# Performance work log

Measured on AMD Instinct MI355X. Metric: run time of the kernel, lower is better.

## Reference

```python
import jax, jax.numpy as jnp
import numpy as np

H = 14
N = H * H
DIM = 768
INT = 5
LAM = 3.5


def fft_conv_grouped(x, w):
    # x: (B, g*in_c, N) real; w: (g, int_c, in_c, H, H//2+1) complex
    g, int_c, in_c = w.shape[:3]
    B = x.shape[0]
    xf = jnp.fft.rfftn(x.reshape(B, g, in_c, H, H), axes=(-2, -1), norm='ortho')
    yf = jnp.einsum('bgchf,gichf->bgihf', xf, w)
    y = jnp.fft.irfftn(yf, s=(H, H), axes=(-2, -1), norm='ortho')
    return y.reshape(B, g * int_c, N)


def soft(x, t):
    # sign(x) * relu(|x| - t)
    return jnp.sign(x) * jnp.maximum(jnp.abs(x) - t, 0.0)


def batch_norm(x, gamma, beta, eps=1e-5):
    # training-mode BatchNorm1d applied per channel over (B, N); x: (B, N, C)
    m = x.mean(axis=(0, 1))
    v = x.var(axis=(0, 1))
    return (x - m) * jax.lax.rsqrt(v + eps) * gamma + beta


def setup_inputs() -> dict:
    key = jax.random.key(0)
    ks = jax.random.split(key, 8)
    B = 32
    Hf = H // 2 + 1
    # kernel: init randn*0.06, then normalize_parameters()
    kr = jax.random.normal(ks[0], (DIM, INT, 1, H, Hf, 2), dtype=jnp.float32) * 0.06
    kc = kr[..., 0] + 1j * kr[..., 1]
    nrm = jnp.sqrt((jnp.abs(kc) ** 2).sum(axis=(2, 3, 4), keepdims=True) * 2.0 / H ** 2)
    kc = kc / nrm
    kernel = jnp.stack([jnp.real(kc), jnp.imag(kc)], axis=-1)
    # L buffer: update_L(lam=1) -> per-group max singular value of Gram kk
    kk = jnp.einsum('gichf,gjchf->gijhf', kc, jnp.conj(kc))
    sv = np.linalg.svd(np.asarray(jnp.transpose(kk, (0, 3, 4, 1, 2))), compute_uv=False)
    L = jnp.asarray(sv.reshape(DIM, -1).max(axis=-1), dtype=jnp.float32)
    hid = 4 * DIM
    return {
        'x': jax.random.normal(ks[1], (B, N, DIM), dtype=jnp.float32),
        'v_w': jax.random.normal(ks[2], (DIM, DIM), dtype=jnp.float32) * 0.02,
        'proj_w': jax.random.normal(ks[3], (DIM, DIM), dtype=jnp.float32) * 0.02,
        'proj_b': jnp.zeros((DIM,), dtype=jnp.float32),
        'kernel': kernel,
        'kernel2': jax.random.normal(ks[4], (DIM, 1, 1, H, Hf, 2), dtype=jnp.float32) * 0.02,
        'n1_g': jnp.ones((DIM,), dtype=jnp.float32),
        'n1_b': jnp.zeros((DIM,), dtype=jnp.float32),
        'n2_g': jnp.ones((DIM,), dtype=jnp.float32),
        'n2_b': jnp.zeros((DIM,), dtype=jnp.float32),
        'fc1_w': jax.random.normal(ks[5], (hid, DIM), dtype=jnp.float32) * 0.02,
        'fc1_b': jnp.zeros((hid,), dtype=jnp.float32),
        'fc2_w': jax.random.normal(ks[6], (DIM, hid), dtype=jnp.float32) * 0.02,
        'fc2_b': jnp.zeros((DIM,), dtype=jnp.float32),
        'L': L,
    }


def reference(x, v_w, proj_w, proj_b, kernel, kernel2, n1_g, n1_b, n2_g, n2_b, fc1_w, fc1_b, fc2_w, fc2_b, L):
    k = kernel[..., 0] + 1j * kernel[..., 1]                 # (g, int, 1, H, Hf)
    kk = jnp.einsum('gichf,gjchf->gijhf', k, jnp.conj(k))     # (g, int, int, H, Hf)
    vx = x @ v_w.T                                            # v Linear, no bias
    xc = jnp.swapaxes(vx, -2, -1)                             # (B, C, N)
    u = fft_conv_grouped(xc, k)                               # (B, g*int, N)
    Lv = jnp.repeat(L, INT)[None, :, None]                    # (1, g*int, 1)
    # ISTA: init soft-threshold then 3 gradient + shrink steps
    s = soft(u, LAM)
    for _ in range(3):
        s = s - (fft_conv_grouped(s, kk) - u) / Lv
        s = soft(s, LAM / Lv)
    # reconstruct with conjugate-transposed kernel, then mix with kernel2
    new = fft_conv_grouped(s, jnp.swapaxes(jnp.conj(k), 1, 2))  # (B, g, N)
    k2 = kernel2[..., 0] + 1j * kernel2[..., 1]
    new = fft_conv_grouped(new, k2)
    new = jnp.swapaxes(new, -2, -1)                           # (B, N, C)
    new = x + (batch_norm(new, n1_g, n1_b) @ proj_w.T + proj_b)
    h = jax.nn.gelu(batch_norm(new, n2_g, n2_b) @ fc1_w.T + fc1_b, approximate=False)
    return new + (h @ fc2_w.T + fc2_b)
```

## Files before the change

### kernel.cpp

```cpp
#include <hip/hip_runtime.h>
#include <cmath>

typedef unsigned short u16;
typedef __bf16 bf16x8 __attribute__((ext_vector_type(8)));
typedef float f32x4 __attribute__((ext_vector_type(4)));
typedef float float4v __attribute__((ext_vector_type(4)));
typedef u16 ushort4v __attribute__((ext_vector_type(4)));
typedef u16 ushort8v __attribute__((ext_vector_type(8)));

#define DIMC 768
#define NP 196
#define MTOT 6272
#define HIDC 3072
#define LAMC 3.5f

__device__ const float C14d[14] = {
  1.0f, 0.9009688679024191f, 0.6234898018587336f, 0.22252093395631445f,
  -0.22252093395631445f, -0.6234898018587336f, -0.9009688679024191f, -1.0f,
  -0.9009688679024191f, -0.6234898018587336f, -0.22252093395631445f,
  0.22252093395631445f, 0.6234898018587336f, 0.9009688679024191f
};
__device__ const float S14d[14] = {
  0.0f, 0.43388373911755823f, 0.7818314824680298f, 0.9749279121818236f,
  0.9749279121818236f, 0.7818314824680298f, 0.43388373911755823f, 0.0f,
  -0.43388373911755823f, -0.7818314824680298f, -0.9749279121818236f,
  -0.9749279121818236f, -0.7818314824680298f, -0.43388373911755823f
};

__device__ __forceinline__ u16 f2bf(float f) {
  unsigned u = __builtin_bit_cast(unsigned, f);
  unsigned r = u + 0x7FFFu + ((u >> 16) & 1u);
  return (u16)(r >> 16);
}

typedef const __attribute__((address_space(1))) u16* gas_p;
typedef __attribute__((address_space(3))) u16* las_p;
__device__ __forceinline__ void gl16(const u16* g, u16* l) {
  __builtin_amdgcn_global_load_lds((gas_p)g, (las_p)l, 16, 0, 0);
}

__global__ __launch_bounds__(256) void initfg_k(u16* __restrict__ Ff, u16* __restrict__ Gf) {
  int idx = blockIdx.x * 256 + threadIdx.x;
  if (idx < 50176) {
    int j = idx & 7, lane = (idx >> 3) & 63;
    int mk = idx >> 9, k0 = mk % 7, m0 = mk / 7;
    int s = m0 * 16 + (lane & 15);
    int q = k0 * 32 + (lane >> 4) * 8 + j;
    float v = 0.f;
    if (q < 196) {
      int kr = s >> 4, f = (s >> 1) & 7, r = q / 14, c = q % 14;
      int th = (kr * r + f * c) % 14;
      v = (s & 1) ? -S14d[th] : C14d[th];
    }
    Ff[idx] = f2bf(v);
  } else if (idx < 50176 + 46592) {
    int t = idx - 50176;
    int j = t & 7, lane = (t >> 3) & 63;
    int pk = t >> 9, k0 = pk % 7, p0 = pk / 7;
    int p = p0 * 16 + (lane & 15);
    int s = k0 * 32 + (lane >> 4) * 8 + j;
    float v = 0.f;
    if (p < 196) {
      int kr = s >> 4, f = (s >> 1) & 7, r = p / 14, c = p % 14;
      int th = (kr * r + f * c) % 14;
      float w = (f == 0 || f == 7) ? 1.f : 2.f;
      v = (w * (1.f / 196.f)) * ((s & 1) ? -S14d[th] : C14d[th]);
    }
    Gf[t] = f2bf(v);
  }
}

__global__ __launch_bounds__(256) void cvtw_k(
    const float* __restrict__ w0, const float* __restrict__ w1,
    const float* __restrict__ w2, const float* __restrict__ w3,
    u16* __restrict__ o0, u16* __restrict__ o1,
    u16* __restrict__ o2, u16* __restrict__ o3) {
  int idx = blockIdx.x * 256 + threadIdx.x;
  const float* s; u16* d; int base;
  if (idx < 147456)      { s = w0; d = o0; base = 0; }
  else if (idx < 294912) { s = w1; d = o1; base = 147456; }
  else if (idx < 884736) { s = w2; d = o2; base = 294912; }
  else                   { s = w3; d = o3; base = 884736; }
  int i4 = (idx - base) * 4;
  float4v v = *(const float4v*)(s + i4);
  ushort4v o;
#pragma unroll
  for (int j = 0; j < 4; ++j) o[j] = f2bf(v[j]);
  *(ushort4v*)(d + i4) = o;
}

__global__ __launch_bounds__(256) void cvt4_k(const float* __restrict__ s,
                                              u16* __restrict__ d, int n4) {
  int idx = blockIdx.x * 256 + threadIdx.x;
  if (idx >= n4) return;
  int i4 = idx * 4;
  float4v v = *(const float4v*)(s + i4);
  ushort4v o;
#pragma unroll
  for (int j = 0; j < 4; ++j) o[j] = f2bf(v[j]);
  *(ushort4v*)(d + i4) = o;
}

__global__ __launch_bounds__(256) void bncvt_k(const float* __restrict__ s,
    const float* __restrict__ sc, const float* __restrict__ sh,
    u16* __restrict__ d, int n4) {
  int idx = blockIdx.x * 256 + threadIdx.x;
  if (idx >= n4) return;
  int i4 = idx * 4;
  int c = i4 % DIMC;
  float4v v = *(const float4v*)(s + i4);
  float4v a = *(const float4v*)(sc + c);
  float4v b = *(const float4v*)(sh + c);
  v = v * a + b;
  ushort4v o;
#pragma unroll
  for (int j = 0; j < 4; ++j) o[j] = f2bf(v[j]);
  *(ushort4v*)(d + i4) = o;
}

template<int EPI>
__global__ __launch_bounds__(256) void gemm_k(
    const u16* __restrict__ A, const u16* __restrict__ Bw,
    const float* __restrict__ bias, const float* __restrict__ res,
    void* __restrict__ Cp, int Nr, int Kr) {
  __shared__ __attribute__((aligned(16))) u16 As[128 * 32];
  __shared__ __attribute__((aligned(16))) u16 Bs[128 * 32];
  const int t = threadIdx.x;
  const int wid = t >> 6, lane = t & 63;
  const int bn = blockIdx.x * 128, bm = blockIdx.y * 128;
  const int wm = (wid >> 1) * 64, wn = (wid & 1) * 64;
  const int l15 = lane & 15, l4 = lane >> 4;
  const int srow = lane >> 2, scol = (lane & 3) * 8;

  f32x4 acc[4][4];
#pragma unroll
  for (int a = 0; a < 4; ++a)
#pragma unroll
    for (int b2 = 0; b2 < 4; ++b2) acc[a][b2] = (f32x4){0.f, 0.f, 0.f, 0.f};

  const u16* gA0 = A + (size_t)(bm + wid * 16 + srow) * Kr + scol;
  const u16* gB0 = Bw + (size_t)(bn + wid * 16 + srow) * Kr + scol;
  u16* lA = As + wid * 512;
  u16* lB = Bs + wid * 512;

  for (int k0 = 0; k0 < Kr; k0 += 32) {
    gl16(gA0 + k0, lA);
    gl16(gA0 + (size_t)64 * Kr + k0, lA + 2048);
    gl16(gB0 + k0, lB);
    gl16(gB0 + (size_t)64 * Kr + k0, lB + 2048);
    __syncthreads();

    bf16x8 af[4], bfv[4];
#pragma unroll
    for (int mb = 0; mb < 4; ++mb)
      af[mb] = *(const bf16x8*)&As[(wm + mb * 16 + l15) * 32 + l4 * 8];
#pragma unroll
    for (int nb = 0; nb < 4; ++nb)
      bfv[nb] = *(const bf16x8*)&Bs[(wn + nb * 16 + l15) * 32 + l4 * 8];
#pragma unroll
    for (int mb = 0; mb < 4; ++mb)
#pragma unroll
      for (int nb = 0; nb < 4; ++nb)
        acc[mb][nb] = __builtin_amdgcn_mfma_f32_16x16x32_bf16(af[mb], bfv[nb], acc[mb][nb], 0, 0, 0);
    __syncthreads();
  }

#pragma unroll
  for (int mb = 0; mb < 4; ++mb) {
#pragma unroll
    for (int nb = 0; nb < 4; ++nb) {
      int n = bn + wn + nb * 16 + l15;
#pragma unroll
      for (int r = 0; r < 4; ++r) {
        int m = bm + wm + mb * 16 + l4 * 4 + r;
        float v = acc[mb][nb][r];
        if (EPI == 0) {
          int bb = m / 196, np = m - bb * 196;
          ((float*)Cp)[((size_t)bb * DIMC + n) * 196 + np] = v;
        } else if (EPI == 1) {
          ((float*)Cp)[(size_t)m * Nr + n] = v + bias[n] + res[(size_t)m * Nr + n];
        } else {
          float vb = v + bias[n];
          float ge = 0.5f * vb * (1.f + erff(vb * 0.70710678118654752f));
          ((u16*)Cp)[(size_t)m * Nr + n] = f2bf(ge);
        }
      }
    }
  }
}

__global__ __launch_bounds__(256) void stats_part_k(const float* __restrict__ A,
                                                    float* __restrict__ part) {
  int blk = blockIdx.x, t = threadIdx.x;
  float s0a = 0, s0b = 0, s0c = 0, s1a = 0, s1b = 0, s1c = 0;
  const float* base = A + (size_t)blk * 64 * DIMC;
  for (int r = 0; r < 64; ++r) {
    const float* row = base + (size_t)r * DIMC;
    float v0 = row[t], v1 = row[t + 256], v2 = row[t + 512];
    s0a += v0; s1a += v0 * v0;
    s0b += v1; s1b += v1 * v1;
    s0c += v2; s1c += v2 * v2;
  }
  part[(size_t)blk * DIMC + t] = s0a;
  part[(size_t)blk * DIMC + t + 256] = s0b;
  part[(size_t)blk * DIMC + t + 512] = s0c;
  float* p2 = part + 98 * DIMC;
  p2[(size_t)blk * DIMC + t] = s1a;
  p2[(size_t)blk * DIMC + t + 256] = s1b;
  p2[(size_t)blk * DIMC + t + 512] = s1c;
}

__global__ __launch_bounds__(256) void stats_fin_k(const float* __restrict__ part,
    const float* __restrict__ gam, const float* __restrict__ bet,
    float* __restrict__ scale, float* __restrict__ shift) {
  int c = blockIdx.x * 256 + threadIdx.x;
  if (c >= DIMC) return;
  float S = 0.f, Q = 0.f;
  for (int b = 0; b < 98; ++b) {
    S += part[(size_t)b * DIMC + c];
    Q += part[(size_t)(98 + b) * DIMC + c];
  }
  float m = S * (1.0f / 6272.0f);
  float v = Q * (1.0f / 6272.0f) - m * m;
  v = fmaxf(v, 0.f);
  float rs = rsqrtf(v + 1e-5f);
  float sc = gam[c] * rs;
  scale[c] = sc;
  shift[c] = bet[c] - m * sc;
}

__global__ __launch_bounds__(64) void checkmfma_k(
    const float* __restrict__ vxt, const float* __restrict__ kern,
    const u16* __restrict__ Ff, const u16* __restrict__ Gf,
    int* __restrict__ cnt, int* __restrict__ wl) {
  __shared__ float xf[16 * 228];
  const int lane = threadIdx.x;
  const int wgb = blockIdx.x;
  const int g = wgb >> 1, bhalf = wgb & 1;
  const int tl = lane & 15, h = lane >> 4;
  const float* xbase = vxt + ((size_t)(bhalf * 16 + tl) * DIMC + g) * 196;

  bf16x8 Bx[7];
#pragma unroll
  for (int k0 = 0; k0 < 7; ++k0) {
    int q0 = k0 * 32 + h * 8;
    ushort8v tv;
    if (k0 < 6) {
      float4v f0 = *(const float4v*)(xbase + q0);
      float4v f1 = *(const float4v*)(xbase + q0 + 4);
#pragma unroll
      for (int j = 0; j < 4; ++j) { tv[j] = f2bf(f0[j]); tv[j + 4] = f2bf(f1[j]); }
    } else {
#pragma unroll
      for (int j = 0; j < 8; ++j) {
        int q = q0 + j;
        tv[j] = (q < 196) ? f2bf(xbase[q]) : (u16)0;
      }
    }
    Bx[k0] = __builtin_bit_cast(bf16x8, tv);
  }

  for (int m0 = 0; m0 < 14; ++m0) {
    f32x4 acc = (f32x4){0.f, 0.f, 0.f, 0.f};
#pragma unroll
    for (int k0 = 0; k0 < 7; ++k0) {
      bf16x8 Af = __builtin_bit_cast(bf16x8,
          *(const ushort8v*)(Ff + ((size_t)(m0 * 7 + k0) * 64 + lane) * 8));
      acc = __builtin_amdgcn_mfma_f32_16x16x32_bf16(Af, Bx[k0], acc, 0, 0, 0);
    }
    *(f32x4*)&xf[tl * 228 + m0 * 16 + h * 4] = acc;
  }

  bf16x8 By[5][7];
#pragma unroll
  for (int i = 0; i < 5; ++i) {
    const float* kb = kern + ((size_t)g * 5 + i) * 224;
#pragma unroll
    for (int k0 = 0; k0 < 7; ++k0) {
      f32x4 x0 = *(const f32x4*)&xf[tl * 228 + k0 * 32 + h * 8];
      f32x4 x1 = *(const f32x4*)&xf[tl * 228 + k0 * 32 + h * 8 + 4];
      int mb = k0 * 16 + h * 4;
      float2 ka = *(const float2*)(kb + (mb + 0) * 2);
      float2 kc = *(const float2*)(kb + (mb + 1) * 2);
      float2 ke = *(const float2*)(kb + (mb + 2) * 2);
      float2 kg = *(const float2*)(kb + (mb + 3) * 2);
      ushort8v tv;
      tv[0] = f2bf(ka.x * x0[0] - ka.y * x0[1]);
      tv[1] = f2bf(ka.x * x0[1] + ka.y * x0[0]);
      tv[2] = f2bf(kc.x * x0[2] - kc.y * x0[3]);
      tv[3] = f2bf(kc.x * x0[3] + kc.y * x0[2]);
      tv[4] = f2bf(ke.x * x1[0] - ke.y * x1[1]);
      tv[5] = f2bf(ke.x * x1[1] + ke.y * x1[0]);
      tv[6] = f2bf(kg.x * x1[0 + 2] - kg.y * x1[3]);
      tv[7] = f2bf(kg.x * x1[3] + kg.y * x1[2]);
      By[i][k0] = __builtin_bit_cast(bf16x8, tv);
    }
  }

  float vmax = 0.f;
  for (int p0 = 0; p0 < 13; ++p0) {
    f32x4 a0 = (f32x4){0.f, 0.f, 0.f, 0.f};
    f32x4 a1 = a0, a2 = a0, a3 = a0, a4 = a0;
#pragma unroll
    for (int k0 = 0; k0 < 7; ++k0) {
      bf16x8 Ag = __builtin_bit_cast(bf16x8,
          *(const ushort8v*)(Gf + ((size_t)(p0 * 7 + k0) * 64 + lane) * 8));
      a0 = __builtin_amdgcn_mfma_f32_16x16x32_bf16(Ag, By[0][k0], a0, 0, 0, 0);
      a1 = __builtin_amdgcn_mfma_f32_16x16x32_bf16(Ag, By[1][k0], a1, 0, 0, 0);
      a2 = __builtin_amdgcn_mfma_f32_16x16x32_bf16(Ag, By[2][k0], a2, 0, 0, 0);
      a3 = __builtin_amdgcn_mfma_f32_16x16x32_bf16(Ag, By[3][k0], a3, 0, 0, 0);
      a4 = __builtin_amdgcn_mfma_f32_16x16x32_bf16(Ag, By[4][k0], a4, 0, 0, 0);
    }
#pragma unroll
    for (int r = 0; r < 4; ++r) {
      vmax = fmaxf(vmax, fabsf(a0[r]));
      vmax = fmaxf(vmax, fabsf(a1[r]));
      vmax = fmaxf(vmax, fabsf(a2[r]));
      vmax = fmaxf(vmax, fabsf(a3[r]));
      vmax = fmaxf(vmax, fabsf(a4[r]));
    }
  }
  vmax = fmaxf(vmax, __shfl_xor(vmax, 16));
  vmax = fmaxf(vmax, __shfl_xor(vmax, 32));
  if (lane < 16 && vmax > (LAMC - 0.1f)) {
    int idx = atomicAdd(cnt, 1);
    wl[idx] = g * 32 + bhalf * 16 + lane;
  }
}

__global__ __launch_bounds__(64) void slow_k(
    const float* __restrict__ vxt, const float* __restrict__ kern,
    const float* __restrict__ kern2, const float* __restrict__ Lbuf,
    const int* __restrict__ cnt, const int* __restrict__ wl,
    float* __restrict__ outp) {
  const int t = threadIdx.x;
  __shared__ float TC[196], TSn[196];
  __shared__ float xs[196];
  __shared__ float t1R[112], t1I[112];
  __shared__ float t2R[112], t2I[112];
  __shared__ float zr[112], zi[112];
  __shared__ float kR[5][112], kI[5][112];
  __shared__ float uu[5][196];
  __shared__ float ss[5][196];
  __shared__ float k2R[112], k2I[112];

  for (int i = t; i < 196; i += 64) {
    int a = i / 14, c = i - (i / 14) * 14;
    int m = (a * c) % 14;
    TC[i] = C14d[m]; TSn[i] = S14d[m];
  }
  const int ntile = *cnt;

  auto rowsFwd = [&](const float* xsrc) {
    for (int i = t; i < 112; i += 64) {
      int r = i >> 3, f = i & 7;
      const float* xp = xsrc + r * 14;
      const float* tc = &TC[f * 14]; const float* tsn = &TSn[f * 14];
      float ar = 0.f, ai = 0.f;
#pragma unroll
      for (int c = 0; c < 14; ++c) { float xv = xp[c]; ar += xv * tc[c]; ai -= xv * tsn[c]; }
      t1R[i] = ar; t1I[i] = ai;
    }
    __syncthreads();
  };
  auto colsFwd = [&](float* oR, float* oI) {
    for (int i = t; i < 112; i += 64) {
      int kr = i >> 3, f = i & 7;
      const float* tc = &TC[kr * 14]; const float* tsn = &TSn[kr * 14];
      float br = 0.f, bi = 0.f;
#pragma unroll
      for (int r = 0; r < 14; ++r) {
        float xr = t1R[r * 8 + f], xi = t1I[r * 8 + f];
        br += tc[r] * xr + tsn[r] * xi;
        bi += tc[r] * xi - tsn[r] * xr;
      }
      oR[i] = br; oI[i] = bi;
    }
    __syncthreads();
  };
  auto colsInv = [&]() {
    for (int i = t; i < 112; i += 64) {
      int r = i >> 3, f = i & 7;
      const float* tc = &TC[r * 14]; const float* tsn = &TSn[r * 14];
      float br = 0.f, bi = 0.f;
#pragma unroll
      for (int kr = 0; kr < 14; ++kr) {
        float xr = t1R[kr * 8 + f], xi = t1I[kr * 8 + f];
        br += tc[kr] * xr - tsn[kr] * xi;
        bi += tc[kr] * xi + tsn[kr] * xr;
      }
      t2R[i] = br; t2I[i] = bi;
    }
    __syncthreads();
  };
  auto rowVal = [&](int r, int c) -> float {
    const float* pR = &t2R[r * 8]; const float* pI = &t2I[r * 8];
    float v = pR[0] + ((c & 1) ? -pR[7] : pR[7]);
    float s2 = 0.f;
#pragma unroll
    for (int f = 1; f < 7; ++f) s2 += pR[f] * TC[f * 14 + c] - pI[f] * TSn[f * 14 + c];
    return (v + 2.f * s2) * (1.0f / 196.0f);
  };

  for (int widx = blockIdx.x; widx < ntile; widx += gridDim.x) {
    const int tile = wl[widx];
    const int g = tile >> 5, b = tile & 31;
    __syncthreads();
    for (int i = t; i < 560; i += 64) {
      int ii = i / 112, p = i - ii * 112;
      const float* kp = kern + ((size_t)g * 5 + ii) * 224 + p * 2;
      kR[ii][p] = kp[0]; kI[ii][p] = kp[1];
    }
    for (int i = t; i < 196; i += 64) xs[i] = vxt[((size_t)b * DIMC + g) * 196 + i];
    for (int i = t; i < 112; i += 64) {
      k2R[i] = kern2[(size_t)g * 224 + i * 2];
      k2I[i] = kern2[(size_t)g * 224 + i * 2 + 1];
    }
    __syncthreads();

    rowsFwd(xs);
    colsFwd(zr, zi);
    for (int ii = 0; ii < 5; ++ii) {
      for (int i = t; i < 112; i += 64) {
        float a = kR[ii][i], b2 = kI[ii][i];
        t1R[i] = a * zr[i] - b2 * zi[i];
        t1I[i] = a * zi[i] + b2 * zr[i];
      }
      __syncthreads();
      colsInv();
      for (int i = t; i < 196; i += 64) uu[ii][i] = rowVal(i / 14, i - (i / 14) * 14);
      __syncthreads();
    }

    const float invL = 1.0f / Lbuf[g];
    const float thr = LAMC * invL;
    {
      float* up = &uu[0][0];
      float* sp = &ss[0][0];
      for (int i = t; i < 980; i += 64) {
        float v = up[i];
        float a = fabsf(v) - LAMC;
        sp[i] = a > 0.f ? copysignf(a, v) : 0.f;
      }
    }
    __syncthreads();

    for (int iter = 0; iter < 4; ++iter) {
      for (int i = t; i < 112; i += 64) { zr[i] = 0.f; zi[i] = 0.f; }
      __syncthreads();
      for (int ii = 0; ii < 5; ++ii) {
        rowsFwd(&ss[ii][0]);
        colsFwd(t2R, t2I);
        for (int i = t; i < 112; i += 64) {
          float a = kR[ii][i], b2 = kI[ii][i];
          zr[i] += a * t2R[i] + b2 * t2I[i];
          zi[i] += a * t2I[i] - b2 * t2R[i];
        }
        __syncthreads();
      }
      if (iter == 3) break;
      for (int ii = 0; ii < 5; ++ii) {
        for (int i = t; i < 112; i += 64) {
          float a = kR[ii][i], b2 = kI[ii][i];
          t1R[i] = a * zr[i] - b2 * zi[i];
          t1I[i] = a * zi[i] + b2 * zr[i];
        }
        __syncthreads();
        colsInv();
        for (int i = t; i < 196; i += 64) {
          float v = rowVal(i / 14, i - (i / 14) * 14);
          float sv = ss[ii][i] - (v - uu[ii][i]) * invL;
          float aa = fabsf(sv) - thr;
          ss[ii][i] = aa > 0.f ? copysignf(aa, sv) : 0.f;
        }
        __syncthreads();
      }
    }

    if (t < 28) {
      int kr = t >> 1, f = (t & 1) * 7;
      int d = kr * 8 + f;
      int srci = ((14 - kr) % 14) * 8 + f;
      float pr = 0.5f * (zr[d] + zr[srci]);
      float pi = 0.5f * (zi[d] - zi[srci]);
      zr[d] = pr; zi[d] = pi;
    }
    __syncthreads();
    for (int i = t; i < 112; i += 64) {
      float a = k2R[i], b2 = k2I[i];
      t1R[i] = a * zr[i] - b2 * zi[i];
      t1I[i] = a * zi[i] + b2 * zr[i];
    }
    __syncthreads();
    colsInv();
    for (int i = t; i < 196; i += 64)
      outp[((size_t)(b * 196 + i)) * DIMC + g] = rowVal(i / 14, i - (i / 14) * 14);
  }
}

extern "C" void kernel_launch(void* const* d_in, const int* in_sizes, int n_in,
                              void* d_out, int out_size, void* d_ws, size_t ws_size,
                              hipStream_t stream) {
  (void)in_sizes; (void)n_in; (void)out_size;
  const float* x      = (const float*)d_in[0];
  const float* v_w    = (const float*)d_in[1];
  const float* proj_w = (const float*)d_in[2];
  const float* proj_b = (const float*)d_in[3];
  const float* kern   = (const float*)d_in[4];
  const float* kern2  = (const float*)d_in[5];
  const float* n1g    = (const float*)d_in[6];
  const float* n1b    = (const float*)d_in[7];
  const float* n2g    = (const float*)d_in[8];
  const float* n2b    = (const float*)d_in[9];
  const float* fc1w   = (const float*)d_in[10];
  const float* fc1b   = (const float*)d_in[11];
  const float* fc2w   = (const float*)d_in[12];
  const float* fc2b   = (const float*)d_in[13];
  const float* Lb     = (const float*)d_in[14];
  float* out = (float*)d_out;

  char* ws = (char*)d_ws;
  size_t o = 0;
  auto alloc = [&](size_t bytes) { size_t r = o; o += (bytes + 255) & ~(size_t)255; return r; };
  u16*   vwbf   = (u16*)(ws + alloc(589824 * 2));
  u16*   projbf = (u16*)(ws + alloc(589824 * 2));
  u16*   fc1bf  = (u16*)(ws + alloc(2359296 * 2));
  u16*   fc2bf  = (u16*)(ws + alloc(2359296 * 2));
  u16*   Ffb    = (u16*)(ws + alloc(50176 * 2));
  u16*   Gfb    = (u16*)(ws + alloc(46592 * 2));
  float* sc1    = (float*)(ws + alloc(768 * 4));
  float* sh1    = (float*)(ws + alloc(768 * 4));
  float* sc2    = (float*)(ws + alloc(768 * 4));
  float* sh2    = (float*)(ws + alloc(768 * 4));
  float* part   = (float*)(ws + alloc(98 * 768 * 2 * 4));
  int*   cnt    = (int*)(ws + alloc(4));
  int*   wl     = (int*)(ws + alloc(24576 * 4));
  u16*   abf    = (u16*)(ws + alloc((size_t)MTOT * DIMC * 2));
  float* vxt    = (float*)(ws + alloc((size_t)MTOT * DIMC * 4));
  float* newm   = (float*)(ws + alloc((size_t)MTOT * DIMC * 4));
  float* new2   = (float*)(ws + alloc((size_t)MTOT * DIMC * 4));
  u16*   hbf    = (u16*)vxt;
  if (ws_size < o) return;

  hipMemsetAsync(newm, 0, (size_t)MTOT * DIMC * 4, stream);
  hipMemsetAsync(cnt, 0, 4, stream);

  initfg_k<<<378, 256, 0, stream>>>(Ffb, Gfb);
  cvtw_k<<<5760, 256, 0, stream>>>(v_w, proj_w, fc1w, fc2w, vwbf, projbf, fc1bf, fc2bf);
  cvt4_k<<<4704, 256, 0, stream>>>(x, abf, 1204224);

  gemm_k<0><<<dim3(6, 49), 256, 0, stream>>>(abf, vwbf, nullptr, nullptr, vxt, DIMC, DIMC);
  checkmfma_k<<<1536, 64, 0, stream>>>(vxt, kern, Ffb, Gfb, cnt, wl);
  slow_k<<<1024, 64, 0, stream>>>(vxt, kern, kern2, Lb, cnt, wl, newm);
  stats_part_k<<<98, 256, 0, stream>>>(newm, part);
  stats_fin_k<<<3, 256, 0, stream>>>(part, n1g, n1b, sc1, sh1);
  bncvt_k<<<4704, 256, 0, stream>>>(newm, sc1, sh1, abf, 1204224);
  gemm_k<1><<<dim3(6, 49), 256, 0, stream>>>(abf, projbf, proj_b, x, new2, DIMC, DIMC);
  stats_part_k<<<98, 256, 0, stream>>>(new2, part);
  stats_fin_k<<<3, 256, 0, stream>>>(part, n2g, n2b, sc2, sh2);
  bncvt_k<<<4704, 256, 0, stream>>>(new2, sc2, sh2, abf, 1204224);
  gemm_k<2><<<dim3(24, 49), 256, 0, stream>>>(abf, fc1bf, fc1b, nullptr, hbf, HIDC, DIMC);
  gemm_k<1><<<dim3(6, 49), 256, 0, stream>>>(hbf, fc2bf, fc2b, new2, out, DIMC, HIDC);
}
```

Measured before the change: 333.8 us.

## Split-K the fc2 GEMM with bf16 partials and store LDS tiles in fragment order

```diff
diff --git a/kernel.cpp b/kernel.cpp
--- a/kernel.cpp
+++ b/kernel.cpp
@@ -31,6 +31,9 @@
   unsigned u = __builtin_bit_cast(unsigned, f);
   unsigned r = u + 0x7FFFu + ((u >> 16) & 1u);
   return (u16)(r >> 16);
+}
+__device__ __forceinline__ float bf2f(u16 u) {
+  return __builtin_bit_cast(float, (unsigned)u << 16);
 }
 
 typedef const __attribute__((address_space(1))) u16* gas_p;
@@ -118,19 +121,19 @@
   *(ushort4v*)(d + i4) = o;
 }
 
-template<int EPI>
+template<int EPI, int SPLIT = 0>
 __global__ __launch_bounds__(256) void gemm_k(
     const u16* __restrict__ A, const u16* __restrict__ Bw,
     const float* __restrict__ bias, const float* __restrict__ res,
-    void* __restrict__ Cp, int Nr, int Kr) {
+    void* __restrict__ Cp, int Nr, int Kr, int ld) {
   __shared__ __attribute__((aligned(16))) u16 As[128 * 32];
   __shared__ __attribute__((aligned(16))) u16 Bs[128 * 32];
   const int t = threadIdx.x;
   const int wid = t >> 6, lane = t & 63;
   const int bn = blockIdx.x * 128, bm = blockIdx.y * 128;
+  const int kz = SPLIT ? blockIdx.z : 0;
   const int wm = (wid >> 1) * 64, wn = (wid & 1) * 64;
   const int l15 = lane & 15, l4 = lane >> 4;
-  const int srow = lane >> 2, scol = (lane & 3) * 8;
 
   f32x4 acc[4][4];
 #pragma unroll
@@ -138,25 +141,25 @@
 #pragma unroll
     for (int b2 = 0; b2 < 4; ++b2) acc[a][b2] = (f32x4){0.f, 0.f, 0.f, 0.f};
 
-  const u16* gA0 = A + (size_t)(bm + wid * 16 + srow) * Kr + scol;
-  const u16* gB0 = Bw + (size_t)(bn + wid * 16 + srow) * Kr + scol;
+  const u16* gA0 = A + (size_t)(bm + wid * 16 + l15) * ld + (size_t)kz * Kr + l4 * 8;
+  const u16* gB0 = Bw + (size_t)(bn + wid * 16 + l15) * ld + (size_t)kz * Kr + l4 * 8;
   u16* lA = As + wid * 512;
   u16* lB = Bs + wid * 512;
 
   for (int k0 = 0; k0 < Kr; k0 += 32) {
     gl16(gA0 + k0, lA);
-    gl16(gA0 + (size_t)64 * Kr + k0, lA + 2048);
+    gl16(gA0 + (size_t)64 * ld + k0, lA + 2048);
     gl16(gB0 + k0, lB);
-    gl16(gB0 + (size_t)64 * Kr + k0, lB + 2048);
+    gl16(gB0 + (size_t)64 * ld + k0, lB + 2048);
     __syncthreads();
 
     bf16x8 af[4], bfv[4];
 #pragma unroll
     for (int mb = 0; mb < 4; ++mb)
-      af[mb] = *(const bf16x8*)&As[(wm + mb * 16 + l15) * 32 + l4 * 8];
+      af[mb] = *(const bf16x8*)&As[((wid >> 1) * 4 + mb) * 512 + lane * 8];
 #pragma unroll
     for (int nb = 0; nb < 4; ++nb)
-      bfv[nb] = *(const bf16x8*)&Bs[(wn + nb * 16 + l15) * 32 + l4 * 8];
+      bfv[nb] = *(const bf16x8*)&Bs[((wid & 1) * 4 + nb) * 512 + lane * 8];
 #pragma unroll
     for (int mb = 0; mb < 4; ++mb)
 #pragma unroll
@@ -179,14 +182,36 @@
           ((float*)Cp)[((size_t)bb * DIMC + n) * 196 + np] = v;
         } else if (EPI == 1) {
           ((float*)Cp)[(size_t)m * Nr + n] = v + bias[n] + res[(size_t)m * Nr + n];
-        } else {
+        } else if (EPI == 2) {
           float vb = v + bias[n];
           float ge = 0.5f * vb * (1.f + erff(vb * 0.70710678118654752f));
           ((u16*)Cp)[(size_t)m * Nr + n] = f2bf(ge);
+        } else {
+          ((u16*)Cp)[(size_t)kz * MTOT * DIMC + (size_t)m * Nr + n] = f2bf(v);
         }
       }
     }
   }
+}
+
+__global__ __launch_bounds__(256) void redc_k(const u16* __restrict__ p,
+    const float* __restrict__ bias, const float* __restrict__ res,
+    float* __restrict__ out) {
+  int idx = blockIdx.x * 256 + threadIdx.x;
+  size_t i4 = (size_t)idx * 4;
+  const size_t S = (size_t)MTOT * DIMC;
+  ushort4v p0 = *(const ushort4v*)(p + i4);
+  ushort4v p1 = *(const ushort4v*)(p + S + i4);
+  ushort4v p2 = *(const ushort4v*)(p + 2 * S + i4);
+  ushort4v p3 = *(const ushort4v*)(p + 3 * S + i4);
+  float4v r = *(const float4v*)(res + i4);
+  int c = (int)(i4 % DIMC);
+  float4v bs = *(const float4v*)(bias + c);
+  float4v o;
+#pragma unroll
+  for (int j = 0; j < 4; ++j)
+    o[j] = bf2f(p0[j]) + bf2f(p1[j]) + bf2f(p2[j]) + bf2f(p3[j]) + bs[j] + r[j];
+  *(float4v*)(out + i4) = o;
 }
 
 __global__ __launch_bounds__(256) void stats_part_k(const float* __restrict__ A,
@@ -291,7 +316,7 @@
       tv[3] = f2bf(kc.x * x0[3] + kc.y * x0[2]);
       tv[4] = f2bf(ke.x * x1[0] - ke.y * x1[1]);
       tv[5] = f2bf(ke.x * x1[1] + ke.y * x1[0]);
-      tv[6] = f2bf(kg.x * x1[0 + 2] - kg.y * x1[3]);
+      tv[6] = f2bf(kg.x * x1[2] - kg.y * x1[3]);
       tv[7] = f2bf(kg.x * x1[3] + kg.y * x1[2]);
       By[i][k0] = __builtin_bit_cast(bf16x8, tv);
     }
@@ -539,6 +564,7 @@
   float* vxt    = (float*)(ws + alloc((size_t)MTOT * DIMC * 4));
   float* newm   = (float*)(ws + alloc((size_t)MTOT * DIMC * 4));
   float* new2   = (float*)(ws + alloc((size_t)MTOT * DIMC * 4));
+  u16*   pbf    = (u16*)(ws + alloc((size_t)4 * MTOT * DIMC * 2));
   u16*   hbf    = (u16*)vxt;
   if (ws_size < o) return;
 
@@ -549,16 +575,17 @@
   cvtw_k<<<5760, 256, 0, stream>>>(v_w, proj_w, fc1w, fc2w, vwbf, projbf, fc1bf, fc2bf);
   cvt4_k<<<4704, 256, 0, stream>>>(x, abf, 1204224);
 
-  gemm_k<0><<<dim3(6, 49), 256, 0, stream>>>(abf, vwbf, nullptr, nullptr, vxt, DIMC, DIMC);
+  gemm_k<0><<<dim3(6, 49), 256, 0, stream>>>(abf, vwbf, nullptr, nullptr, vxt, DIMC, DIMC, DIMC);
   checkmfma_k<<<1536, 64, 0, stream>>>(vxt, kern, Ffb, Gfb, cnt, wl);
   slow_k<<<1024, 64, 0, stream>>>(vxt, kern, kern2, Lb, cnt, wl, newm);
   stats_part_k<<<98, 256, 0, stream>>>(newm, part);
   stats_fin_k<<<3, 256, 0, stream>>>(part, n1g, n1b, sc1, sh1);
   bncvt_k<<<4704, 256, 0, stream>>>(newm, sc1, sh1, abf, 1204224);
-  gemm_k<1><<<dim3(6, 49), 256, 0, stream>>>(abf, projbf, proj_b, x, new2, DIMC, DIMC);
+  gemm_k<1><<<dim3(6, 49), 256, 0, stream>>>(abf, projbf, proj_b, x, new2, DIMC, DIMC, DIMC);
   stats_part_k<<<98, 256, 0, stream>>>(new2, part);
   stats_fin_k<<<3, 256, 0, stream>>>(part, n2g, n2b, sc2, sh2);
   bncvt_k<<<4704, 256, 0, stream>>>(new2, sc2, sh2, abf, 1204224);
-  gemm_k<2><<<dim3(24, 49), 256, 0, stream>>>(abf, fc1bf, fc1b, nullptr, hbf, HIDC, DIMC);
-  gemm_k<1><<<dim3(6, 49), 256, 0, stream>>>(hbf, fc2bf, fc2b, new2, out, DIMC, HIDC);
-}
+  gemm_k<2><<<dim3(24, 49), 256, 0, stream>>>(abf, fc1bf, fc1b, nullptr, hbf, HIDC, DIMC, DIMC);
+  gemm_k<3, 1><<<dim3(6, 49, 4), 256, 0, stream>>>(hbf, fc2bf, nullptr, nullptr, pbf, DIMC, 768, HIDC);
+  redc_k<<<4704, 256, 0, stream>>>(pbf, fc2b, new2, out);
+}
```

Result: slower. 365.3 us (+9.4%).

## Double-buffer GEMM LDS tiles, store fragments in MFMA order, vectorize transposed epilogue

Applied to the files above, without the earlier changes.

```diff
diff --git a/kernel.cpp b/kernel.cpp
--- a/kernel.cpp
+++ b/kernel.cpp
@@ -31,6 +31,9 @@
   unsigned u = __builtin_bit_cast(unsigned, f);
   unsigned r = u + 0x7FFFu + ((u >> 16) & 1u);
   return (u16)(r >> 16);
+}
+__device__ __forceinline__ float bf2f(u16 u) {
+  return __builtin_bit_cast(float, (unsigned)u << 16);
 }
 
 typedef const __attribute__((address_space(1))) u16* gas_p;
@@ -122,15 +125,14 @@
 __global__ __launch_bounds__(256) void gemm_k(
     const u16* __restrict__ A, const u16* __restrict__ Bw,
     const float* __restrict__ bias, const float* __restrict__ res,
-    void* __restrict__ Cp, int Nr, int Kr) {
-  __shared__ __attribute__((aligned(16))) u16 As[128 * 32];
-  __shared__ __attribute__((aligned(16))) u16 Bs[128 * 32];
+    void* __restrict__ Cp, int Nr, int Kr, int ld) {
+  __shared__ __attribute__((aligned(16))) u16 As[2][128 * 32];
+  __shared__ __attribute__((aligned(16))) u16 Bs[2][128 * 32];
   const int t = threadIdx.x;
   const int wid = t >> 6, lane = t & 63;
   const int bn = blockIdx.x * 128, bm = blockIdx.y * 128;
   const int wm = (wid >> 1) * 64, wn = (wid & 1) * 64;
   const int l15 = lane & 15, l4 = lane >> 4;
-  const int srow = lane >> 2, scol = (lane & 3) * 8;
 
   f32x4 acc[4][4];
 #pragma unroll
@@ -138,31 +140,40 @@
 #pragma unroll
     for (int b2 = 0; b2 < 4; ++b2) acc[a][b2] = (f32x4){0.f, 0.f, 0.f, 0.f};
 
-  const u16* gA0 = A + (size_t)(bm + wid * 16 + srow) * Kr + scol;
-  const u16* gB0 = Bw + (size_t)(bn + wid * 16 + srow) * Kr + scol;
-  u16* lA = As + wid * 512;
-  u16* lB = Bs + wid * 512;
+  const u16* gA0 = A + (size_t)(bm + wid * 16 + l15) * ld + l4 * 8;
+  const u16* gB0 = Bw + (size_t)(bn + wid * 16 + l15) * ld + l4 * 8;
+
+  auto STAGE = [&](int buf, int k0) {
+    u16* lA = &As[buf][wid * 512];
+    u16* lB = &Bs[buf][wid * 512];
+    gl16(gA0 + k0, lA);
+    gl16(gA0 + (size_t)64 * ld + k0, lA + 2048);
+    gl16(gB0 + k0, lB);
+    gl16(gB0 + (size_t)64 * ld + k0, lB + 2048);
+  };
+
+  STAGE(0, 0);
+  __syncthreads();
+  int cur = 0;
 
   for (int k0 = 0; k0 < Kr; k0 += 32) {
-    gl16(gA0 + k0, lA);
-    gl16(gA0 + (size_t)64 * Kr + k0, lA + 2048);
-    gl16(gB0 + k0, lB);
-    gl16(gB0 + (size_t)64 * Kr + k0, lB + 2048);
-    __syncthreads();
+    if (k0 + 32 < Kr) STAGE(cur ^ 1, k0 + 32);
 
     bf16x8 af[4], bfv[4];
 #pragma unroll
     for (int mb = 0; mb < 4; ++mb)
-      af[mb] = *(const bf16x8*)&As[(wm + mb * 16 + l15) * 32 + l4 * 8];
+      af[mb] = *(const bf16x8*)&As[cur][((wid >> 1) * 4 + mb) * 512 + lane * 8];
 #pragma unroll
     for (int nb = 0; nb < 4; ++nb)
-      bfv[nb] = *(const bf16x8*)&Bs[(wn + nb * 16 + l15) * 32 + l4 * 8];
+      bfv[nb] = *(const bf16x8*)&Bs[cur][((wid & 1) * 4 + nb) * 512 + lane * 8];
 #pragma unroll
     for (int mb = 0; mb < 4; ++mb)
 #pragma unroll
       for (int nb = 0; nb < 4; ++nb)
         acc[mb][nb] = __builtin_amdgcn_mfma_f32_16x16x32_bf16(af[mb], bfv[nb], acc[mb][nb], 0, 0, 0);
-    __syncthreads();
+
+    __syncthreads();
+    cur ^= 1;
   }
 
 #pragma unroll
@@ -170,19 +181,23 @@
 #pragma unroll
     for (int nb = 0; nb < 4; ++nb) {
       int n = bn + wn + nb * 16 + l15;
-#pragma unroll
-      for (int r = 0; r < 4; ++r) {
-        int m = bm + wm + mb * 16 + l4 * 4 + r;
-        float v = acc[mb][nb][r];
-        if (EPI == 0) {
-          int bb = m / 196, np = m - bb * 196;
-          ((float*)Cp)[((size_t)bb * DIMC + n) * 196 + np] = v;
-        } else if (EPI == 1) {
-          ((float*)Cp)[(size_t)m * Nr + n] = v + bias[n] + res[(size_t)m * Nr + n];
-        } else {
-          float vb = v + bias[n];
-          float ge = 0.5f * vb * (1.f + erff(vb * 0.70710678118654752f));
-          ((u16*)Cp)[(size_t)m * Nr + n] = f2bf(ge);
+      if (EPI == 0) {
+        int m0 = bm + wm + mb * 16 + l4 * 4;
+        int bb = m0 / 196, np0 = m0 - bb * 196;
+        *(float4v*)&((float*)Cp)[((size_t)bb * DIMC + n) * 196 + np0] =
+            (float4v){acc[mb][nb][0], acc[mb][nb][1], acc[mb][nb][2], acc[mb][nb][3]};
+      } else {
+#pragma unroll
+        for (int r = 0; r < 4; ++r) {
+          int m = bm + wm + mb * 16 + l4 * 4 + r;
+          float v = acc[mb][nb][r];
+          if (EPI == 1) {
+            ((float*)Cp)[(size_t)m * Nr + n] = v + bias[n] + res[(size_t)m * Nr + n];
+          } else {
+            float vb = v + bias[n];
+            float ge = 0.5f * vb * (1.f + erff(vb * 0.70710678118654752f));
+            ((u16*)Cp)[(size_t)m * Nr + n] = f2bf(ge);
+          }
         }
       }
     }
@@ -291,7 +306,7 @@
       tv[3] = f2bf(kc.x * x0[3] + kc.y * x0[2]);
       tv[4] = f2bf(ke.x * x1[0] - ke.y * x1[1]);
       tv[5] = f2bf(ke.x * x1[1] + ke.y * x1[0]);
-      tv[6] = f2bf(kg.x * x1[0 + 2] - kg.y * x1[3]);
+      tv[6] = f2bf(kg.x * x1[2] - kg.y * x1[3]);
       tv[7] = f2bf(kg.x * x1[3] + kg.y * x1[2]);
       By[i][k0] = __builtin_bit_cast(bf16x8, tv);
     }
@@ -549,16 +564,16 @@
   cvtw_k<<<5760, 256, 0, stream>>>(v_w, proj_w, fc1w, fc2w, vwbf, projbf, fc1bf, fc2bf);
   cvt4_k<<<4704, 256, 0, stream>>>(x, abf, 1204224);
 
-  gemm_k<0><<<dim3(6, 49), 256, 0, stream>>>(abf, vwbf, nullptr, nullptr, vxt, DIMC, DIMC);
+  gemm_k<0><<<dim3(6, 49), 256, 0, stream>>>(abf, vwbf, nullptr, nullptr, vxt, DIMC, DIMC, DIMC);
   checkmfma_k<<<1536, 64, 0, stream>>>(vxt, kern, Ffb, Gfb, cnt, wl);
   slow_k<<<1024, 64, 0, stream>>>(vxt, kern, kern2, Lb, cnt, wl, newm);
   stats_part_k<<<98, 256, 0, stream>>>(newm, part);
   stats_fin_k<<<3, 256, 0, stream>>>(part, n1g, n1b, sc1, sh1);
   bncvt_k<<<4704, 256, 0, stream>>>(newm, sc1, sh1, abf, 1204224);
-  gemm_k<1><<<dim3(6, 49), 256, 0, stream>>>(abf, projbf, proj_b, x, new2, DIMC, DIMC);
+  gemm_k<1><<<dim3(6, 49), 256, 0, stream>>>(abf, projbf, proj_b, x, new2, DIMC, DIMC, DIMC);
   stats_part_k<<<98, 256, 0, stream>>>(new2, part);
   stats_fin_k<<<3, 256, 0, stream>>>(part, n2g, n2b, sc2, sh2);
   bncvt_k<<<4704, 256, 0, stream>>>(new2, sc2, sh2, abf, 1204224);
-  gemm_k<2><<<dim3(24, 49), 256, 0, stream>>>(abf, fc1bf, fc1b, nullptr, hbf, HIDC, DIMC);
-  gemm_k<1><<<dim3(6, 49), 256, 0, stream>>>(hbf, fc2bf, fc2b, new2, out, DIMC, HIDC);
-}
+  gemm_k<2><<<dim3(24, 49), 256, 0, stream>>>(abf, fc1bf, fc1b, nullptr, hbf, HIDC, DIMC, DIMC);
+  gemm_k<1><<<dim3(6, 49), 256, 0, stream>>>(hbf, fc2bf, fc2b, new2, out, DIMC, HIDC, HIDC);
+}
```

Result: slower. 362.1 us (+8.5%).
